# Performance work log

Measured on AMD Instinct MI355X. Metric: run time of the kernel, lower is better.

## Reference

```python
import jax, jax.numpy as jnp
import numpy as np

N = 50000      # total nodes in batched graph
E = 800000     # total edges
G = 512        # number of graphs in the batch
NF = 32        # input node feature dim
EF = 16        # edge feature dim
HID = [64, 128, 128, 256]


def _seg_mean(vals, ids, num):
    s = jax.ops.segment_sum(vals, ids, num_segments=num)
    c = jax.ops.segment_sum(jnp.ones((vals.shape[0], 1), vals.dtype), ids, num_segments=num)
    return s / jnp.maximum(c, 1.0)


def setup_inputs() -> dict:
    key = jax.random.key(0)
    ks = list(jax.random.split(key, 64))
    it = iter(ks)

    def nk():
        return next(it)

    inp = {}
    inp["x"] = jax.random.normal(nk(), (N, NF), jnp.float32)
    inp["e"] = jax.random.normal(nk(), (E, EF), jnp.float32)
    inp["src"] = jax.random.randint(nk(), (E,), 0, N)
    inp["dst"] = jax.random.randint(nk(), (E,), 0, N)
    inp["gid"] = jnp.sort(jax.random.randint(nk(), (N,), 0, G))
    fin = NF
    for i, f in enumerate(HID):
        inp[f"Wm{i}"] = jax.random.normal(nk(), (fin + EF, f), jnp.float32) / np.sqrt(fin + EF)
        inp[f"bm{i}"] = jnp.zeros((f,), jnp.float32)
        inp[f"Ws{i}"] = jax.random.normal(nk(), (fin, f), jnp.float32) / np.sqrt(fin)
        inp[f"bs{i}"] = jnp.zeros((f,), jnp.float32)
        inp[f"Wc{i}"] = jax.random.normal(nk(), (f, 1), jnp.float32) / np.sqrt(f)
        inp[f"bc{i}"] = jnp.zeros((1,), jnp.float32)
        fin = f
    return inp


def _molconv(x, e, src, dst, Wm, bm, Ws, bs):
    # gather source node feats, condition on edge feats, per-edge MLP
    m = jax.nn.relu(jnp.concatenate([x[src], e], axis=-1) @ Wm + bm)  # [E, out]
    agg = _seg_mean(m, dst, x.shape[0])                               # scatter-mean to dst
    return jax.nn.relu(agg + x @ Ws + bs)                             # [N, out]


def reference(x, e, src, dst, gid,
              Wm0, bm0, Ws0, bs0, Wc0, bc0,
              Wm1, bm1, Ws1, bs1, Wc1, bc1,
              Wm2, bm2, Ws2, bs2, Wc2, bc2,
              Wm3, bm3, Ws3, bs3, Wc3, bc3):
    layers = [(Wm0, bm0, Ws0, bs0, Wc0, bc0),
              (Wm1, bm1, Ws1, bs1, Wc1, bc1),
              (Wm2, bm2, Ws2, bs2, Wc2, bc2),
              (Wm3, bm3, Ws3, bs3, Wc3, bc3)]
    feat = x
    score = jnp.zeros((G, 1), x.dtype)
    for Wm, bm, Ws, bs, Wc, bc in layers:
        feat = _molconv(feat, e, src, dst, Wm, bm, Ws, bs)
        # per-layer Linear(feats,1) classifier + AvgPooling per graph, summed
        score = score + _seg_mean(feat @ Wc + bc, gid, G)
    return score
```

## Files before the change

### kernel.cpp

```cpp
#include <hip/hip_runtime.h>

#define NN 50000
#define EE 800000
#define GG 512
#define NP 50048
#define EB 3125
#define SCB 196

typedef short bf16x8 __attribute__((ext_vector_type(8)));
typedef float floatx4 __attribute__((ext_vector_type(4)));

__device__ inline unsigned short f2b(float f) {
    unsigned u = __float_as_uint(f);
    unsigned r = (u + 0x7fffu + ((u >> 16) & 1u)) >> 16;
    return (unsigned short)r;
}
__device__ inline float b2f(unsigned short b) {
    return __uint_as_float(((unsigned)b) << 16);
}


__global__ void conv_all(const float* __restrict__ x, unsigned short* __restrict__ xb, long n8x,
                         const float* __restrict__ ef, unsigned short* __restrict__ efB, long n8e) {
    long i = (long)blockIdx.x * blockDim.x + threadIdx.x;
    const float* s;
    unsigned short* d;
    long idx;
    if (i < n8x) { s = x; d = xb; idx = i; }
    else if (i < n8x + n8e) { s = ef; d = efB; idx = i - n8x; }
    else return;
    float4 a = ((const float4*)s)[2 * idx];
    float4 b = ((const float4*)s)[2 * idx + 1];
    unsigned short o[8] = {f2b(a.x), f2b(a.y), f2b(a.z), f2b(a.w),
                           f2b(b.x), f2b(b.y), f2b(b.z), f2b(b.w)};
    ((uint4*)d)[idx] = *(uint4*)o;
}


struct TpD { const float* W; unsigned short* WT; int K, F, Kp, rowOff; };
struct TpTab { TpD d[12]; };

__global__ void tp_all(TpTab t) {
    TpD dd = t.d[blockIdx.y];
    int f = blockIdx.x;
    if (f >= dd.F) return;
    for (int k = threadIdx.x; k < dd.Kp; k += blockDim.x)
        dd.WT[(size_t)f * dd.Kp + k] =
            (k < dd.K) ? f2b(dd.W[(size_t)(dd.rowOff + k) * dd.F + f]) : (unsigned short)0;
}


__global__ void hist_cnt(const int* __restrict__ dst, int* __restrict__ hist,
                         const int* __restrict__ gid, float* __restrict__ gcnt) {
    int b = blockIdx.x;
    if (b < EB) {
        int e = b * 256 + threadIdx.x;
        if (e < EE) atomicAdd(&hist[dst[e]], 1);
    } else {
        int n = (b - EB) * 256 + threadIdx.x;
        if (n < NN) atomicAdd(&gcnt[gid[n]], 1.0f);
    }
}

__global__ void scanA(const int* __restrict__ hist, int* __restrict__ bsum) {
    __shared__ int sb[256];
    int idx = blockIdx.x * 256 + threadIdx.x;
    sb[threadIdx.x] = (idx < NN) ? hist[idx] : 0;
    __syncthreads();
    for (int off = 128; off > 0; off >>= 1) {
        if (threadIdx.x < off) sb[threadIdx.x] += sb[threadIdx.x + off];
        __syncthreads();
    }
    if (threadIdx.x == 0) bsum[blockIdx.x] = sb[0];
}

__global__ void scanB(const int* __restrict__ bsum, int* __restrict__ boff) {
    __shared__ int sb[256];
    int t = threadIdx.x;
    int v = (t < SCB) ? bsum[t] : 0;
    sb[t] = v;
    __syncthreads();
    for (int off = 1; off < 256; off <<= 1) {
        int u = (t >= off) ? sb[t - off] : 0;
        __syncthreads();
        sb[t] += u;
        __syncthreads();
    }
    if (t < SCB) boff[t] = sb[t] - v;
}

__global__ void scanC(const int* __restrict__ hist, const int* __restrict__ boff,
                      int* __restrict__ cursor, float* __restrict__ invdeg,
                      float* __restrict__ gcnt, float* __restrict__ score,
                      const float* __restrict__ bc0, const float* __restrict__ bc1,
                      const float* __restrict__ bc2, const float* __restrict__ bc3) {
    __shared__ int sb[256];
    int t = threadIdx.x;
    int idx = blockIdx.x * 256 + t;
    int v = (idx < NN) ? hist[idx] : 0;
    sb[t] = v;
    __syncthreads();
    for (int off = 1; off < 256; off <<= 1) {
        int u = (t >= off) ? sb[t - off] : 0;
        __syncthreads();
        sb[t] += u;
        __syncthreads();
    }
    if (idx < NN) {
        cursor[idx] = boff[blockIdx.x] + sb[t] - v;
        invdeg[idx] = 1.0f / fmaxf((float)v, 1.0f);
    }
    if (idx < GG) {
        float c = gcnt[idx];
        gcnt[idx] = 1.0f / fmaxf(c, 1.0f);
        score[idx] = (c > 0.0f) ? (bc0[0] + bc1[0] + bc2[0] + bc3[0]) : 0.0f;
    }
}

__global__ void scatter_kernel(const int* __restrict__ src, const int* __restrict__ dst,
                               int* __restrict__ cursor, const unsigned short* __restrict__ efB,
                               int* __restrict__ srcS, int* __restrict__ dstS,
                               unsigned short* __restrict__ efS) {
    int e = blockIdx.x * blockDim.x + threadIdx.x;
    if (e < EE) {
        int d = dst[e];
        int p = atomicAdd(&cursor[d], 1);
        srcS[p] = src[e];
        dstS[p] = d;
        const uint4* s = (const uint4*)&efB[(size_t)e * 16];
        uint4* dd = (uint4*)&efS[(size_t)p * 16];
        dd[0] = s[0];
        dd[1] = s[1];
    }
}


template<int FIN, int F>
__global__ __launch_bounds__(256)
void nodeP(const unsigned short* __restrict__ featB, const unsigned short* __restrict__ WxT,
           unsigned short* __restrict__ P, float* __restrict__ agg)
{
    const int tid = threadIdx.x;
    const int w   = tid >> 6;
    const int l   = tid & 63;
    const int l16 = l & 15;
    const int q   = l >> 4;
    const int cb  = blockIdx.y * 64;
    const int nb  = blockIdx.x * 64;
    const int row = nb + w * 16 + l16;

    {
        const int zr = nb + (tid >> 4);
        const int zc = cb + ((tid & 15) << 2);
        const float4 z4 = {0.f, 0.f, 0.f, 0.f};
        #pragma unroll
        for (int i = 0; i < 4; ++i) {
            int n = zr + i * 16;
            if (n < NN) *(float4*)&agg[(size_t)n * F + zc] = z4;
        }
    }

    floatx4 acc[4];
    #pragma unroll
    for (int nt = 0; nt < 4; ++nt) acc[nt] = (floatx4){0.f, 0.f, 0.f, 0.f};

    #pragma unroll
    for (int kb = 0; kb < FIN; kb += 32) {
        bf16x8 a = *(const bf16x8*)&featB[(size_t)row * FIN + kb + q * 8];
        #pragma unroll
        for (int nt = 0; nt < 4; ++nt) {
            bf16x8 b = *(const bf16x8*)&WxT[(size_t)(cb + nt * 16 + l16) * FIN + kb + q * 8];
            acc[nt] = __builtin_amdgcn_mfma_f32_16x16x32_bf16(a, b, acc[nt], 0, 0, 0);
        }
    }

    #pragma unroll
    for (int nt = 0; nt < 4; ++nt)
        #pragma unroll
        for (int r = 0; r < 4; ++r) {
            int ro = nb + w * 16 + q * 4 + r;
            P[(size_t)ro * F + cb + nt * 16 + l16] = f2b(acc[nt][r]);
        }
}


#define RXO(r) ((((r) >> 2 & 1) << 4) | (((r) >> 3 & 1) << 3))

template<int F>
__global__ __launch_bounds__(256, 4)
void edge_q(const unsigned short* __restrict__ efS,
            const int* __restrict__ srcS, const int* __restrict__ dstS,
            const unsigned short* __restrict__ WeT, const unsigned short* __restrict__ P,
            const float* __restrict__ bm, float* __restrict__ agg)
{
    constexpr int CW  = (F >= 128) ? 128 : 64;
    constexpr int WPG = F / CW;
    constexpr int NT  = CW / 16;
    constexpr int EPB = 64 * (4 / WPG);
    constexpr int RS  = CW;

    __shared__ __align__(16) float red[4][16 * RS];

    const int tid = threadIdx.x;
    const int w   = tid >> 6;
    const int l   = tid & 63;
    const int l16 = l & 15;
    const int q   = l >> 4;
    const int sub = w / WPG;
    const int cb  = (w % WPG) * CW;
    const int be  = blockIdx.x * EPB + sub * 64;

    const int dreg = dstS[be + l];
    const int sreg = srcS[be + l];

    const bf16x8 ZV = {0, 0, 0, 0, 0, 0, 0, 0};
    const int xo = ((q & 1) << 4) | ((q >> 1) << 3);
    float* redw = &red[w][0];

    bf16x8 bfr[NT];
    #pragma unroll
    for (int nt = 0; nt < NT; ++nt)
        bfr[nt] = *(const bf16x8*)&WeT[(size_t)(cb + nt * 16 + l16) * 32 + q * 8];

    if constexpr (CW == 128) {
        float2 bmv;
        bmv.x = bm[cb + 2 * l];
        bmv.y = bm[cb + 2 * l + 1];

        int cur_d = -1;
        float2 csum = {0.f, 0.f};
        bool from_start = false;

        bf16x8 a_cur = ZV, a_nxt;
        if (q < 2) a_cur = *(const bf16x8*)&efS[(size_t)(be + l16) * 16 + q * 8];
        unsigned pvv[16], pvn[16];
        #pragma unroll
        for (int r = 0; r < 16; ++r) {
            int sr = __shfl(sreg, r);
            pvv[r] = *(const unsigned*)&P[(size_t)sr * F + cb + 2 * l];
        }

        #pragma unroll
        for (int mt = 0; mt < 4; ++mt) {
            if (mt < 3) {
                a_nxt = ZV;
                if (q < 2) a_nxt = *(const bf16x8*)&efS[(size_t)(be + (mt + 1) * 16 + l16) * 16 + q * 8];
            }
            #pragma unroll
            for (int nt = 0; nt < NT; ++nt) {
                floatx4 acc = __builtin_amdgcn_mfma_f32_16x16x32_bf16(
                    a_cur, bfr[nt], (floatx4){0.f, 0.f, 0.f, 0.f}, 0, 0, 0);
                #pragma unroll
                for (int r4 = 0; r4 < 4; ++r4)
                    redw[(q * 4 + r4) * RS + ((nt * 16 + l16) ^ xo)] = acc[r4];
            }
            if (mt < 3) {
                #pragma unroll
                for (int r = 0; r < 16; ++r) {
                    int sr = __shfl(sreg, (mt + 1) * 16 + r);
                    pvn[r] = *(const unsigned*)&P[(size_t)sr * F + cb + 2 * l];
                }
                __builtin_amdgcn_sched_barrier(0);
            }
            #pragma unroll
            for (int r = 0; r < 16; ++r) {
                int gr = mt * 16 + r;
                int d = __shfl(dreg, gr);
                float2 qv = *(const float2*)&redw[r * RS + ((2 * l) ^ RXO(r))];
                float2 v;
                v.x = fmaxf(qv.x + __uint_as_float(pvv[r] << 16)          + bmv.x, 0.f);
                v.y = fmaxf(qv.y + __uint_as_float(pvv[r] & 0xffff0000u) + bmv.y, 0.f);
                if (gr == 0) {
                    cur_d = d; csum = v; from_start = true;
                } else if (d != cur_d) {
                    float* ap = &agg[(size_t)cur_d * F + cb + 2 * l];
                    if (from_start) { atomicAdd(ap, csum.x); atomicAdd(ap + 1, csum.y); }
                    else            { *(float2*)ap = csum; }
                    cur_d = d; csum = v; from_start = false;
                } else {
                    csum.x += v.x; csum.y += v.y;
                }
            }
            if (mt < 3) {
                #pragma unroll
                for (int r = 0; r < 16; ++r) pvv[r] = pvn[r];
                a_cur = a_nxt;
            }
        }
        float* ap = &agg[(size_t)cur_d * F + cb + 2 * l];
        atomicAdd(ap, csum.x);
        atomicAdd(ap + 1, csum.y);
    } else {
        const float bmv = bm[cb + l];

        int cur_d = -1;
        float csum = 0.f;
        bool from_start = false;

        bf16x8 a_cur = ZV, a_nxt;
        if (q < 2) a_cur = *(const bf16x8*)&efS[(size_t)(be + l16) * 16 + q * 8];
        float pvv[16], pvn[16];
        #pragma unroll
        for (int r = 0; r < 16; ++r) {
            int sr = __shfl(sreg, r);
            pvv[r] = b2f(P[(size_t)sr * F + cb + l]);
        }

        #pragma unroll
        for (int mt = 0; mt < 4; ++mt) {
            if (mt < 3) {
                a_nxt = ZV;
                if (q < 2) a_nxt = *(const bf16x8*)&efS[(size_t)(be + (mt + 1) * 16 + l16) * 16 + q * 8];
            }
            #pragma unroll
            for (int nt = 0; nt < NT; ++nt) {
                floatx4 acc = __builtin_amdgcn_mfma_f32_16x16x32_bf16(
                    a_cur, bfr[nt], (floatx4){0.f, 0.f, 0.f, 0.f}, 0, 0, 0);
                #pragma unroll
                for (int r4 = 0; r4 < 4; ++r4)
                    redw[(q * 4 + r4) * RS + ((nt * 16 + l16) ^ xo)] = acc[r4];
            }
            if (mt < 3) {
                #pragma unroll
                for (int r = 0; r < 16; ++r) {
                    int sr = __shfl(sreg, (mt + 1) * 16 + r);
                    pvn[r] = b2f(P[(size_t)sr * F + cb + l]);
                }
                __builtin_amdgcn_sched_barrier(0);
            }
            #pragma unroll
            for (int r = 0; r < 16; ++r) {
                int gr = mt * 16 + r;
                int d = __shfl(dreg, gr);
                float qv = redw[r * RS + (l ^ RXO(r))];
                float v = fmaxf(qv + pvv[r] + bmv, 0.f);
                if (gr == 0) {
                    cur_d = d; csum = v; from_start = true;
                } else if (d != cur_d) {
                    float* ap = &agg[(size_t)cur_d * F + cb + l];
                    if (from_start) atomicAdd(ap, csum);
                    else *ap = csum;
                    cur_d = d; csum = v; from_start = false;
                } else {
                    csum += v;
                }
            }
            if (mt < 3) {
                #pragma unroll
                for (int r = 0; r < 16; ++r) pvv[r] = pvn[r];
                a_cur = a_nxt;
            }
        }
        atomicAdd(&agg[(size_t)cur_d * F + cb + l], csum);
    }
}


template<int FIN, int F>
__global__ __launch_bounds__(256)
void node_mfma(const unsigned short* __restrict__ featB, const float* __restrict__ agg,
               const unsigned short* __restrict__ WsT, const float* __restrict__ bs,
               const float* __restrict__ Wc, const float* __restrict__ invdeg,
               unsigned short* __restrict__ fout, float* __restrict__ rd)
{
    const int tid = threadIdx.x;
    const int w   = tid >> 6;
    const int l   = tid & 63;
    const int l16 = l & 15;
    const int q   = l >> 4;
    const int cb  = blockIdx.y * 64;
    const int nb  = blockIdx.x * 64;
    const int row = nb + w * 16 + l16;

    floatx4 acc[4];
    #pragma unroll
    for (int nt = 0; nt < 4; ++nt) acc[nt] = (floatx4){0.f, 0.f, 0.f, 0.f};

    #pragma unroll
    for (int kb = 0; kb < FIN; kb += 32) {
        bf16x8 a = *(const bf16x8*)&featB[(size_t)row * FIN + kb + q * 8];
        #pragma unroll
        for (int nt = 0; nt < 4; ++nt) {
            bf16x8 b = *(const bf16x8*)&WsT[(size_t)(cb + nt * 16 + l16) * FIN + kb + q * 8];
            acc[nt] = __builtin_amdgcn_mfma_f32_16x16x32_bf16(a, b, acc[nt], 0, 0, 0);
        }
    }

    float wcv[4], bsv[4];
    #pragma unroll
    for (int nt = 0; nt < 4; ++nt) {
        wcv[nt] = Wc[cb + nt * 16 + l16];
        bsv[nt] = bs[cb + nt * 16 + l16];
    }

    #pragma unroll
    for (int r = 0; r < 4; ++r) {
        int n = nb + w * 16 + q * 4 + r;
        bool valid = n < NN;
        float idg = valid ? invdeg[n] : 0.f;
        float s = 0.f;
        #pragma unroll
        for (int nt = 0; nt < 4; ++nt) {
            int col = cb + nt * 16 + l16;
            float av = valid ? agg[(size_t)n * F + col] : 0.f;
            float v = fmaxf(acc[nt][r] + av * idg + bsv[nt], 0.f);
            if (valid) fout[(size_t)n * F + col] = f2b(v);
            s += v * wcv[nt];
        }
        s += __shfl_xor(s, 1);
        s += __shfl_xor(s, 2);
        s += __shfl_xor(s, 4);
        s += __shfl_xor(s, 8);
        if (valid && l16 == 0) atomicAdd(&rd[n], s);
    }
}


__global__ void score_reduce(const float* __restrict__ rd, const int* __restrict__ gid,
                             const float* __restrict__ invg, float* __restrict__ score) {
    int n = blockIdx.x * blockDim.x + threadIdx.x;
    int l = threadIdx.x & 63;
    bool valid = n < NN;
    int g = valid ? gid[n] : -1;
    float v = valid ? rd[n] : 0.f;
    #pragma unroll
    for (int off = 1; off < 64; off <<= 1) {
        float vo = __shfl_up(v, off);
        int go = __shfl_up(g, off);
        if (l >= off && go == g) v += vo;
    }
    int gn = __shfl_down(g, 1);
    bool tail = (l == 63) || (gn != g);
    if (valid && tail) atomicAdd(&score[g], v * invg[g]);
}


extern "C" void kernel_launch(void* const* d_in, const int* in_sizes, int n_in,
                              void* d_out, int out_size, void* d_ws, size_t ws_size,
                              hipStream_t stream) {
    const float* x   = (const float*)d_in[0];
    const float* ef  = (const float*)d_in[1];
    const int*   src = (const int*)d_in[2];
    const int*   dst = (const int*)d_in[3];
    const int*   gid = (const int*)d_in[4];
    const float *Wm[4], *bm[4], *Ws[4], *bs[4], *Wc[4], *bc[4];
    for (int i = 0; i < 4; ++i) {
        Wm[i] = (const float*)d_in[5 + 6 * i];
        bm[i] = (const float*)d_in[6 + 6 * i];
        Ws[i] = (const float*)d_in[7 + 6 * i];
        bs[i] = (const float*)d_in[8 + 6 * i];
        Wc[i] = (const float*)d_in[9 + 6 * i];
        bc[i] = (const float*)d_in[10 + 6 * i];
    }

    char* w = (char*)d_ws;
    float* agg = (float*)w;                  w += (size_t)NN * 256 * 4;
    unsigned short* xb  = (unsigned short*)w; w += (size_t)NP * 32 * 2;
    unsigned short* f1  = (unsigned short*)w; w += (size_t)NP * 64 * 2;
    unsigned short* f2  = (unsigned short*)w; w += (size_t)NP * 128 * 2;
    unsigned short* f3  = (unsigned short*)w; w += (size_t)NP * 128 * 2;
    unsigned short* f4  = (unsigned short*)w; w += (size_t)NP * 256 * 2;
    unsigned short* P   = (unsigned short*)w; w += (size_t)NP * 256 * 2;
    unsigned short* efB = (unsigned short*)w; w += (size_t)EE * 16 * 2;
    unsigned short* efS = (unsigned short*)w; w += (size_t)EE * 16 * 2;
    unsigned short* WxT0 = (unsigned short*)w; w += (size_t)64 * 32 * 2;
    unsigned short* WxT1 = (unsigned short*)w; w += (size_t)128 * 64 * 2;
    unsigned short* WxT2 = (unsigned short*)w; w += (size_t)128 * 128 * 2;
    unsigned short* WxT3 = (unsigned short*)w; w += (size_t)256 * 128 * 2;
    unsigned short* WeT0 = (unsigned short*)w; w += (size_t)64 * 32 * 2;
    unsigned short* WeT1 = (unsigned short*)w; w += (size_t)128 * 32 * 2;
    unsigned short* WeT2 = (unsigned short*)w; w += (size_t)128 * 32 * 2;
    unsigned short* WeT3 = (unsigned short*)w; w += (size_t)256 * 32 * 2;
    unsigned short* WsT0 = (unsigned short*)w; w += (size_t)64 * 32 * 2;
    unsigned short* WsT1 = (unsigned short*)w; w += (size_t)128 * 64 * 2;
    unsigned short* WsT2 = (unsigned short*)w; w += (size_t)128 * 128 * 2;
    unsigned short* WsT3 = (unsigned short*)w; w += (size_t)256 * 128 * 2;
    float* invdeg = (float*)w;               w += (size_t)NN * 4;
    float* invg   = (float*)w;               w += (size_t)GG * 4;
    float* rd     = (float*)w;               w += (size_t)NN * 4;
    int* hist   = (int*)w;                   w += (size_t)(NN + 1) * 4;
    int* srcS   = (int*)w;                   w += (size_t)EE * 4;
    int* dstS   = (int*)w;                   w += (size_t)EE * 4;
    int* bsum   = (int*)w;                   w += (size_t)SCB * 4;
    int* boff   = (int*)w;                   w += (size_t)SCB * 4;
    int* cursor = (int*)w;                   w += (size_t)NN * 4;
    float* score = (float*)d_out;

    const long n8x = (long)NN * 32 / 8, n8e = (long)EE * 16 / 8;
    conv_all<<<(n8x + n8e + 255) / 256, 256, 0, stream>>>(x, xb, n8x, ef, efB, n8e);

    TpTab tt;
    tt.d[0]  = {Wm[0], WxT0,  32,  64,  32,   0};
    tt.d[1]  = {Wm[1], WxT1,  64, 128,  64,   0};
    tt.d[2]  = {Wm[2], WxT2, 128, 128, 128,   0};
    tt.d[3]  = {Wm[3], WxT3, 128, 256, 128,   0};
    tt.d[4]  = {Wm[0], WeT0,  16,  64,  32,  32};
    tt.d[5]  = {Wm[1], WeT1,  16, 128,  32,  64};
    tt.d[6]  = {Wm[2], WeT2,  16, 128,  32, 128};
    tt.d[7]  = {Wm[3], WeT3,  16, 256,  32, 128};
    tt.d[8]  = {Ws[0], WsT0,  32,  64,  32,   0};
    tt.d[9]  = {Ws[1], WsT1,  64, 128,  64,   0};
    tt.d[10] = {Ws[2], WsT2, 128, 128, 128,   0};
    tt.d[11] = {Ws[3], WsT3, 128, 256, 128,   0};
    tp_all<<<dim3(256, 12), 256, 0, stream>>>(tt);

    hipMemsetAsync(invg, 0, (size_t)(GG + NN + NN + 1) * 4, stream);
    hist_cnt<<<EB + SCB, 256, 0, stream>>>(dst, hist, gid, invg);
    scanA<<<SCB, 256, 0, stream>>>(hist, bsum);
    scanB<<<1, 256, 0, stream>>>(bsum, boff);
    scanC<<<SCB, 256, 0, stream>>>(hist, boff, cursor, invdeg, invg, score,
                                   bc[0], bc[1], bc[2], bc[3]);
    scatter_kernel<<<EB, 256, 0, stream>>>(src, dst, cursor, efB, srcS, dstS, efS);

    const int NB = NP / 64;

    nodeP<32, 64><<<dim3(NB, 1), 256, 0, stream>>>(xb, WxT0, P, agg);
    edge_q<64><<<EB, 256, 0, stream>>>(efS, srcS, dstS, WeT0, P, bm[0], agg);
    node_mfma<32, 64><<<dim3(NB, 1), 256, 0, stream>>>(xb, agg, WsT0, bs[0], Wc[0], invdeg, f1, rd);

    nodeP<64, 128><<<dim3(NB, 2), 256, 0, stream>>>(f1, WxT1, P, agg);
    edge_q<128><<<EB, 256, 0, stream>>>(efS, srcS, dstS, WeT1, P, bm[1], agg);
    node_mfma<64, 128><<<dim3(NB, 2), 256, 0, stream>>>(f1, agg, WsT1, bs[1], Wc[1], invdeg, f2, rd);

    nodeP<128, 128><<<dim3(NB, 2), 256, 0, stream>>>(f2, WxT2, P, agg);
    edge_q<128><<<EB, 256, 0, stream>>>(efS, srcS, dstS, WeT2, P, bm[2], agg);
    node_mfma<128, 128><<<dim3(NB, 2), 256, 0, stream>>>(f2, agg, WsT2, bs[2], Wc[2], invdeg, f3, rd);

    nodeP<128, 256><<<dim3(NB, 4), 256, 0, stream>>>(f3, WxT3, P, agg);
    edge_q<256><<<EE / 128, 256, 0, stream>>>(efS, srcS, dstS, WeT3, P, bm[3], agg);
    node_mfma<128, 256><<<dim3(NB, 4), 256, 0, stream>>>(f3, agg, WsT3, bs[3], Wc[3], invdeg, f4, rd);

    score_reduce<<<SCB, 256, 0, stream>>>(rd, gid, invg, score);
}
```

Measured before the change: 717.9 us.

## Gather source-node rows with wide vector loads staged through shared memory

The edge kernel used to fetch source-node projections as 16 narrow per-lane loads per tile. It now fetches each row of 16 edges with 16-byte vector loads, 4 lanes per row, into a swizzled per-wave LDS staging buffer, and then reads from LDS during the reduction. The goal is fewer, wider and more coalesced global gather transactions and lower register pressure. In exchange it adds LDS traffic and footprint, and the launch-bounds occupancy hint drops from 4 to 3 blocks.

```diff
diff --git a/kernel.cpp b/kernel.cpp
--- a/kernel.cpp
+++ b/kernel.cpp
@@ -187,7 +187,7 @@
 #define RXO(r) ((((r) >> 2 & 1) << 4) | (((r) >> 3 & 1) << 3))
 
 template<int F>
-__global__ __launch_bounds__(256, 4)
+__global__ __launch_bounds__(256, 3)
 void edge_q(const unsigned short* __restrict__ efS,
             const int* __restrict__ srcS, const int* __restrict__ dstS,
             const unsigned short* __restrict__ WeT, const unsigned short* __restrict__ P,
@@ -198,8 +198,10 @@
     constexpr int NT  = CW / 16;
     constexpr int EPB = 64 * (4 / WPG);
     constexpr int RS  = CW;
+    constexpr int NL  = CW / 32;
 
     __shared__ __align__(16) float red[4][16 * RS];
+    __shared__ __align__(16) unsigned short stg[4][16 * CW];
 
     const int tid = threadIdx.x;
     const int w   = tid >> 6;
@@ -213,14 +215,32 @@
     const int dreg = dstS[be + l];
     const int sreg = srcS[be + l];
 
+    const int grow = l >> 2;
+    const int gchk = l & 3;
+    const size_t gcol = (size_t)cb + gchk * (NL * 8);
+
     const bf16x8 ZV = {0, 0, 0, 0, 0, 0, 0, 0};
     const int xo = ((q & 1) << 4) | ((q >> 1) << 3);
     float* redw = &red[w][0];
+    unsigned short* stw = &stg[w][0];
 
     bf16x8 bfr[NT];
     #pragma unroll
     for (int nt = 0; nt < NT; ++nt)
         bfr[nt] = *(const bf16x8*)&WeT[(size_t)(cb + nt * 16 + l16) * 32 + q * 8];
+
+    {
+        int srg = __shfl(sreg, grow);
+        const uint4* gp = (const uint4*)&P[(size_t)srg * F + gcol];
+        uint4 gl[NL];
+        #pragma unroll
+        for (int i = 0; i < NL; ++i) gl[i] = gp[i];
+        #pragma unroll
+        for (int i = 0; i < NL; ++i)
+            *(uint4*)&stw[grow * CW + ((gchk * (NL * 8) + i * 8) ^ ((grow & 7) << 3))] = gl[i];
+    }
+    bf16x8 a_cur = ZV, a_nxt;
+    if (q < 2) a_cur = *(const bf16x8*)&efS[(size_t)(be + l16) * 16 + q * 8];
 
     if constexpr (CW == 128) {
         float2 bmv;
@@ -231,20 +251,17 @@
         float2 csum = {0.f, 0.f};
         bool from_start = false;
 
-        bf16x8 a_cur = ZV, a_nxt;
-        if (q < 2) a_cur = *(const bf16x8*)&efS[(size_t)(be + l16) * 16 + q * 8];
-        unsigned pvv[16], pvn[16];
-        #pragma unroll
-        for (int r = 0; r < 16; ++r) {
-            int sr = __shfl(sreg, r);
-            pvv[r] = *(const unsigned*)&P[(size_t)sr * F + cb + 2 * l];
-        }
-
         #pragma unroll
         for (int mt = 0; mt < 4; ++mt) {
+            uint4 gl[NL];
             if (mt < 3) {
+                int srg = __shfl(sreg, (mt + 1) * 16 + grow);
+                const uint4* gp = (const uint4*)&P[(size_t)srg * F + gcol];
+                #pragma unroll
+                for (int i = 0; i < NL; ++i) gl[i] = gp[i];
                 a_nxt = ZV;
                 if (q < 2) a_nxt = *(const bf16x8*)&efS[(size_t)(be + (mt + 1) * 16 + l16) * 16 + q * 8];
+                __builtin_amdgcn_sched_barrier(0);
             }
             #pragma unroll
             for (int nt = 0; nt < NT; ++nt) {
@@ -254,22 +271,15 @@
                 for (int r4 = 0; r4 < 4; ++r4)
                     redw[(q * 4 + r4) * RS + ((nt * 16 + l16) ^ xo)] = acc[r4];
             }
-            if (mt < 3) {
-                #pragma unroll
-                for (int r = 0; r < 16; ++r) {
-                    int sr = __shfl(sreg, (mt + 1) * 16 + r);
-                    pvn[r] = *(const unsigned*)&P[(size_t)sr * F + cb + 2 * l];
-                }
-                __builtin_amdgcn_sched_barrier(0);
-            }
             #pragma unroll
             for (int r = 0; r < 16; ++r) {
                 int gr = mt * 16 + r;
                 int d = __shfl(dreg, gr);
                 float2 qv = *(const float2*)&redw[r * RS + ((2 * l) ^ RXO(r))];
+                unsigned pv = *(const unsigned*)&stw[r * CW + ((2 * l) ^ ((r & 7) << 3))];
                 float2 v;
-                v.x = fmaxf(qv.x + __uint_as_float(pvv[r] << 16)          + bmv.x, 0.f);
-                v.y = fmaxf(qv.y + __uint_as_float(pvv[r] & 0xffff0000u) + bmv.y, 0.f);
+                v.x = fmaxf(qv.x + __uint_as_float(pv << 16)          + bmv.x, 0.f);
+                v.y = fmaxf(qv.y + __uint_as_float(pv & 0xffff0000u) + bmv.y, 0.f);
                 if (gr == 0) {
                     cur_d = d; csum = v; from_start = true;
                 } else if (d != cur_d) {
@@ -283,7 +293,8 @@
             }
             if (mt < 3) {
                 #pragma unroll
-                for (int r = 0; r < 16; ++r) pvv[r] = pvn[r];
+                for (int i = 0; i < NL; ++i)
+                    *(uint4*)&stw[grow * CW + ((gchk * (NL * 8) + i * 8) ^ ((grow & 7) << 3))] = gl[i];
                 a_cur = a_nxt;
             }
         }
@@ -297,20 +308,17 @@
         float csum = 0.f;
         bool from_start = false;
 
-        bf16x8 a_cur = ZV, a_nxt;
-        if (q < 2) a_cur = *(const bf16x8*)&efS[(size_t)(be + l16) * 16 + q * 8];
-        float pvv[16], pvn[16];
-        #pragma unroll
-        for (int r = 0; r < 16; ++r) {
-            int sr = __shfl(sreg, r);
-            pvv[r] = b2f(P[(size_t)sr * F + cb + l]);
-        }
-
         #pragma unroll
         for (int mt = 0; mt < 4; ++mt) {
+            uint4 gl[NL];
             if (mt < 3) {
+                int srg = __shfl(sreg, (mt + 1) * 16 + grow);
+                const uint4* gp = (const uint4*)&P[(size_t)srg * F + gcol];
+                #pragma unroll
+                for (int i = 0; i < NL; ++i) gl[i] = gp[i];
                 a_nxt = ZV;
                 if (q < 2) a_nxt = *(const bf16x8*)&efS[(size_t)(be + (mt + 1) * 16 + l16) * 16 + q * 8];
+                __builtin_amdgcn_sched_barrier(0);
             }
             #pragma unroll
             for (int nt = 0; nt < NT; ++nt) {
@@ -320,20 +328,13 @@
                 for (int r4 = 0; r4 < 4; ++r4)
                     redw[(q * 4 + r4) * RS + ((nt * 16 + l16) ^ xo)] = acc[r4];
             }
-            if (mt < 3) {
-                #pragma unroll
-                for (int r = 0; r < 16; ++r) {
-                    int sr = __shfl(sreg, (mt + 1) * 16 + r);
-                    pvn[r] = b2f(P[(size_t)sr * F + cb + l]);
-                }
-                __builtin_amdgcn_sched_barrier(0);
-            }
             #pragma unroll
             for (int r = 0; r < 16; ++r) {
                 int gr = mt * 16 + r;
                 int d = __shfl(dreg, gr);
                 float qv = redw[r * RS + (l ^ RXO(r))];
-                float v = fmaxf(qv + pvv[r] + bmv, 0.f);
+                float pvf = b2f(stw[r * CW + (l ^ ((r & 7) << 3))]);
+                float v = fmaxf(qv + pvf + bmv, 0.f);
                 if (gr == 0) {
                     cur_d = d; csum = v; from_start = true;
                 } else if (d != cur_d) {
@@ -347,7 +348,8 @@
             }
             if (mt < 3) {
                 #pragma unroll
-                for (int r = 0; r < 16; ++r) pvv[r] = pvn[r];
+                for (int i = 0; i < NL; ++i)
+                    *(uint4*)&stw[grow * CW + ((gchk * (NL * 8) + i * 8) ^ ((grow & 7) << 3))] = gl[i];
                 a_cur = a_nxt;
             }
         }
```

Measured after the change: 784.9 us. 9.3% more time.
